# Kernel tuning notes

Hardware: AMD Instinct MI355X
Metric: run time of the kernel (lower is better)

Reference implementation:

```python
import jax, jax.numpy as jnp
import numpy as np

B, N, C = 4, 2304, 256
H = 8                      # num_heads
D = C // H                 # head_dim = 32
SCALE = D ** -0.5
H_DS, W_DS = 48, 48
UP = 2                     # spatial_down_ratio
EPS = 1e-5


def setup_inputs() -> dict:
    key = jax.random.key(0)
    ks = jax.random.split(key, 16)
    g = lambda k, shape, s: (jax.random.normal(k, shape, dtype=jnp.float32) * s)
    return {
        "x1": g(ks[0], (B, N, C), 1.0),
        "x2": g(ks[1], (B, N, C), 1.0),
        # attention projections (torch Linear convention: [out, in], no bias)
        "q1_w": g(ks[2], (C, C), C ** -0.5),
        "kv1_w": g(ks[3], (2 * C, C), C ** -0.5),
        "q2_w": g(ks[4], (C, C), C ** -0.5),
        "kv2_w": g(ks[5], (2 * C, C), C ** -0.5),
        # per-head scalar biases
        "beta12": jnp.full((H,), 0.2, dtype=jnp.float32),
        "beta21": jnp.full((H,), 0.1, dtype=jnp.float32),
        # output projections
        "p1_w": g(ks[6], (C, C), (2.0 / C) ** 0.5),
        "p1_b": g(ks[7], (C,), 1e-2),
        "p2_w": g(ks[8], (C, C), (2.0 / C) ** 0.5),
        "p2_b": g(ks[9], (C,), 1e-2),
        # LayerNorm affine params
        "g1": jnp.ones((C,), dtype=jnp.float32),
        "b1": jnp.zeros((C,), dtype=jnp.float32),
        "g2": jnp.ones((C,), dtype=jnp.float32),
        "b2": jnp.zeros((C,), dtype=jnp.float32),
    }


def _heads(x):
    # [B,N,C] -> [B,H,N,D]
    return x.reshape(B, N, H, D).transpose(0, 2, 1, 3)


def _merge(x):
    # [B,H,N,D] -> [B,N,C]
    return x.transpose(0, 2, 1, 3).reshape(B, N, C)


def _cross_attn(q, k, v, beta):
    # scores: [B,H,N,N] with per-head scalar bias
    s = jnp.einsum("bhqd,bhkd->bhqk", q, k) * SCALE + beta[None, :, None, None]
    a = jax.nn.softmax(s, axis=-1)
    return jnp.einsum("bhqk,bhkd->bhqd", a, v)


def _layernorm(x, g, b):
    mu = jnp.mean(x, axis=-1, keepdims=True)
    var = jnp.var(x, axis=-1, keepdims=True)
    return (x - mu) * jax.lax.rsqrt(var + EPS) * g + b


def _forward(x1, x2, q1_w, kv1_w, q2_w, kv2_w, beta12, beta21,
             p1_w, p1_b, p2_w, p2_b, g1, b1, g2, b2):
    q1 = _heads(x1 @ q1_w.T)
    kv1 = x1 @ kv1_w.T          # [B,N,2C]
    k1, v1 = _heads(kv1[..., :C]), _heads(kv1[..., C:])
    q2 = _heads(x2 @ q2_w.T)
    kv2 = x2 @ kv2_w.T
    k2, v2 = _heads(kv2[..., :C]), _heads(kv2[..., C:])

    o1 = _merge(_cross_attn(q1, k2, v2, beta12))   # x1 attends to x2
    o2 = _merge(_cross_attn(q2, k1, v1, beta21))   # x2 attends to x1

    y1 = _layernorm(jax.nn.relu(o1 @ p1_w.T + p1_b), g1, b1)
    y2 = _layernorm(jax.nn.relu(o2 @ p2_w.T + p2_b), g2, b2)

    # [B,N,C] -> [B,C,H_ds,W_ds]
    y1 = y1.transpose(0, 2, 1).reshape(B, C, H_DS, W_DS)
    y2 = y2.transpose(0, 2, 1).reshape(B, C, H_DS, W_DS)

    # bilinear upsample x2, align_corners=False (half-pixel == jax.image default)
    out_shape = (B, C, H_DS * UP, W_DS * UP)
    y1 = jax.image.resize(y1, out_shape, method="bilinear")
    y2 = jax.image.resize(y2, out_shape, method="bilinear")
    return y1, y2


def reference(x1, x2, q1_w, kv1_w, q2_w, kv2_w, beta12, beta21,
              p1_w, p1_b, p2_w, p2_b, g1, b1, g2, b2):
    return _forward(x1, x2, q1_w, kv1_w, q2_w, kv2_w, beta12, beta21,
                    p1_w, p1_b, p2_w, p2_b, g1, b1, g2, b2)
```

## Files before the change

kernel.cpp:

```cpp
#include <hip/hip_runtime.h>
#include <math.h>


typedef __attribute__((ext_vector_type(8))) short short8;
typedef __attribute__((ext_vector_type(4))) float f32x4;
typedef __attribute__((ext_vector_type(16))) float f32x16;
typedef __attribute__((ext_vector_type(2))) unsigned uint32x2;

#define MFMA16(a, b, c) __builtin_amdgcn_mfma_f32_16x16x32_bf16((a), (b), (c), 0, 0, 0)
#define MFMA32(a, b, c) __builtin_amdgcn_mfma_f32_32x32x16_bf16((a), (b), (c), 0, 0, 0)

__device__ __forceinline__ float bf2f(ushort u) {
    union { unsigned u; float f; } x; x.u = ((unsigned)u) << 16; return x.f;
}
__device__ __forceinline__ ushort f2bf(float f) {
    union { float f; unsigned u; } x; x.f = f;
    unsigned u = x.u;
    return (ushort)((u + 0x7fffu + ((u >> 16) & 1u)) >> 16);
}
__device__ __forceinline__ unsigned cvt_pk_bf16(float a, float b) {
    unsigned r;
    asm("v_cvt_pk_bf16_f32 %0, %1, %2" : "=v"(r) : "v"(a), "v"(b));
    return r;
}
__device__ __forceinline__ float fast_ex2(float x) {
    float r;
    asm("v_exp_f32 %0, %1" : "=v"(r) : "v"(x));
    return r;
}
__device__ __forceinline__ void plswap(unsigned &a, unsigned &b) {
    uint32x2 r = __builtin_amdgcn_permlane32_swap(a, b, false, false);
    a = r[0]; b = r[1];
}

__global__ void sniff_kernel(const ushort* __restrict__ x, int* __restrict__ flag)
{
    int lane = threadIdx.x;
    ushort u = x[lane * 2];
    int e = (u >> 7) & 0xFF;
    int outlier = (e < 100 || e > 135) ? 1 : 0;
    unsigned long long m = __ballot(outlier);
    if (lane == 0) *flag = (__popcll(m) >= 16) ? 1 : 0;
}

__global__ __launch_bounds__(256) void convert_params(
    const void* s0, const void* s1, const void* s2, const void* s3,
    const void* s4, const void* s5, const void* s6, const void* s7,
    const void* s8, const void* s9, const void* s10, const void* s11,
    ushort* __restrict__ dst, const int* __restrict__ flag)
{
    int idx = blockIdx.x * 256 + threadIdx.x;
    if (idx >= 525824) return;
    const void* src; int off;
    if      (idx < 65536)  { src = s0;  off = idx; }
    else if (idx < 196608) { src = s1;  off = idx - 65536; }
    else if (idx < 262144) { src = s2;  off = idx - 196608; }
    else if (idx < 393216) { src = s3;  off = idx - 262144; }
    else if (idx < 458752) { src = s4;  off = idx - 393216; }
    else if (idx < 524288) { src = s5;  off = idx - 458752; }
    else if (idx < 524544) { src = s6;  off = idx - 524288; }
    else if (idx < 524800) { src = s7;  off = idx - 524544; }
    else if (idx < 525056) { src = s8;  off = idx - 524800; }
    else if (idx < 525312) { src = s9;  off = idx - 525056; }
    else if (idx < 525568) { src = s10; off = idx - 525312; }
    else                   { src = s11; off = idx - 525568; }
    ushort v = (*flag) ? f2bf(((const float*)src)[off])
                       : ((const ushort*)src)[off];
    dst[idx] = v;
}

__global__ __launch_bounds__(256) void convert_x(
    const void* __restrict__ x1, const void* __restrict__ x2,
    ushort* __restrict__ o1, ushort* __restrict__ o2,
    const int* __restrict__ flag)
{
    int idx = blockIdx.x * 256 + threadIdx.x;
    int which = idx >= 294912;
    int off = (which ? idx - 294912 : idx) * 8;
    const void* src = which ? x2 : x1;
    ushort* dst = which ? o2 : o1;
    if (*flag) {
        const float* p = (const float*)src + off;
        float4 a = *(const float4*)p;
        float4 c = *(const float4*)(p + 4);
        uint4 u;
        u.x = cvt_pk_bf16(a.x, a.y);
        u.y = cvt_pk_bf16(a.z, a.w);
        u.z = cvt_pk_bf16(c.x, c.y);
        u.w = cvt_pk_bf16(c.z, c.w);
        *(uint4*)(dst + off) = u;
    } else {
        *(uint4*)(dst + off) = *(const uint4*)((const ushort*)src + off);
    }
}

__global__ __launch_bounds__(256) void gemm_bt(
    const void* __restrict__ Ain, const ushort* __restrict__ W,
    ushort* __restrict__ C, const ushort* __restrict__ bias,
    int M, int N, int K, int relu, const int* __restrict__ dflag, int a_ext,
    int mode, ushort* __restrict__ Kh, ushort* __restrict__ Vt,
    const ushort* __restrict__ W2, const ushort* __restrict__ bias2,
    ushort* __restrict__ Kh2, ushort* __restrict__ Vt2, int mhalf)
{
    __shared__ __align__(16) ushort As[64][40];
    __shared__ __align__(16) ushort Ws[64][40];

    const int m0 = blockIdx.x * 64;
    const int n0 = blockIdx.y * 64;
    const int tid = threadIdx.x;
    const int w = tid >> 6;
    const int lane = tid & 63;
    const int lm = lane & 15;
    const int quad = lane >> 4;
    const int a32 = a_ext ? *dflag : 0;

    const int side = (mhalf && m0 >= mhalf) ? 1 : 0;
    const ushort* Wu = side ? W2 : W;
    const ushort* bu = side ? bias2 : bias;
    ushort* Khu = side ? Kh2 : Kh;
    ushort* Vtu = side ? Vt2 : Vt;

    const f32x4 Z4 = {0.f, 0.f, 0.f, 0.f};
    f32x4 acc[4];
    for (int j = 0; j < 4; j++) acc[j] = Z4;

    const ushort* A16 = (const ushort*)Ain;
    const float*  A32 = (const float*)Ain;
    const int row = tid >> 2, off = (tid & 3) * 8;

    for (int k0 = 0; k0 < K; k0 += 32) {
        __syncthreads();
        if (a32) {
            const float* p0 = A32 + (size_t)(m0 + row) * K + k0 + off;
            float4 f0 = *(const float4*)p0;
            float4 f1 = *(const float4*)(p0 + 4);
            uint4 t0;
            t0.x = cvt_pk_bf16(f0.x, f0.y);
            t0.y = cvt_pk_bf16(f0.z, f0.w);
            t0.z = cvt_pk_bf16(f1.x, f1.y);
            t0.w = cvt_pk_bf16(f1.z, f1.w);
            *(uint4*)&As[row][off] = t0;
        } else {
            *(uint4*)&As[row][off] =
                *(const uint4*)(A16 + (size_t)(m0 + row) * K + k0 + off);
        }
        *(uint4*)&Ws[row][off] =
            *(const uint4*)(Wu + (size_t)(n0 + row) * K + k0 + off);
        __syncthreads();

        short8 af = *(const short8*)&As[w * 16 + lm][quad * 8];
        for (int nt = 0; nt < 4; nt++) {
            short8 wf = *(const short8*)&Ws[nt * 16 + lm][quad * 8];
            acc[nt] = MFMA16(af, wf, acc[nt]);
        }
    }

    const int grow = m0 + w * 16 + quad * 4;
    const int grel = grow - (side ? mhalf : 0);
    if (mode == 1) {
        const float QSC = 0.17677669529663687f * 1.4426950408889634f;
        int bb = grel / 2304;
        int tok = grel - bb * 2304;
        for (int nt = 0; nt < 4; nt++) {
            int col = n0 + nt * 16 + lm;
            if (col < 256) {
                for (int r = 0; r < 4; r++)
                    C[(size_t)(grow + r) * 256 + col] = f2bf(acc[nt][r] * QSC);
            } else if (col < 512) {
                int c2 = col - 256, hh = c2 >> 5, d = c2 & 31;
                size_t kb = ((size_t)(bb * 8 + hh) * 72 + (tok >> 5)) * 1024
                          + (size_t)(d >> 4) * 512 + (size_t)(d & 15);
                for (int r = 0; r < 4; r++)
                    Khu[kb + (size_t)((tok + r) & 31) * 16] = f2bf(acc[nt][r]);
            } else {
                int c2 = col - 512, hh = c2 >> 5, d = c2 & 31;
                size_t vb = ((size_t)(bb * 8 + hh) * 144 + (tok >> 4)) * 512
                          + (size_t)d * 16 + (size_t)(tok & 15);
                uint2 o;
                o.x = cvt_pk_bf16(acc[nt][0], acc[nt][1]);
                o.y = cvt_pk_bf16(acc[nt][2], acc[nt][3]);
                *(uint2*)&Vtu[vb] = o;
            }
        }
    } else {
        for (int nt = 0; nt < 4; nt++) {
            int col = n0 + nt * 16 + lm;
            float bv = bu ? bf2f(bu[col]) : 0.f;
            for (int r = 0; r < 4; r++) {
                float v = acc[nt][r] + bv;
                if (relu) v = fmaxf(v, 0.f);
                C[(size_t)(grow + r) * N + col] = f2bf(v);
            }
        }
    }
}

__global__ __launch_bounds__(256) void attn_kernel(
    const ushort* __restrict__ Qa, const ushort* __restrict__ Kha,
    const ushort* __restrict__ Vta, ushort* __restrict__ Oa,
    const ushort* __restrict__ Qb, const ushort* __restrict__ Khb2,
    const ushort* __restrict__ Vtb2, ushort* __restrict__ Ob)
{
    __shared__ float Lo[4][2][64][16];
    __shared__ float Ll[4][2][64];

    const int sid = blockIdx.x;
    const int qb = blockIdx.y;
    const int side = sid >> 5;
    const int bh = sid & 31;
    const ushort* Q  = side ? Qb   : Qa;
    const ushort* Kh = side ? Khb2 : Kha;
    const ushort* Vt = side ? Vtb2 : Vta;
    ushort* O        = side ? Ob   : Oa;

    const int b = bh >> 3, h = bh & 7;
    const int tid = threadIdx.x;
    const int w = tid >> 6, lane = tid & 63;
    const int l31 = lane & 31, hl = lane >> 5;

    const int qrow0 = qb * 64 + l31;
    const int qrow1 = qrow0 + 32;
    const ushort* qp0 = Q + ((size_t)b * 2304 + qrow0) * 256 + h * 32 + hl * 8;
    const ushort* qp1 = Q + ((size_t)b * 2304 + qrow1) * 256 + h * 32 + hl * 8;
    const short8 qf0a = *(const short8*)qp0;
    const short8 qf1a = *(const short8*)(qp0 + 16);
    const short8 qf0b = *(const short8*)qp1;
    const short8 qf1b = *(const short8*)(qp1 + 16);

    f32x16 oa, ob;
    #pragma unroll
    for (int i = 0; i < 16; i++) { oa[i] = 0.f; ob[i] = 0.f; }
    const f32x16 Z16 = oa;
    float la = 0.f, lb = 0.f;

    const ushort* kp0 = Kh + (size_t)bh * 73728 + l31 * 16 + hl * 8;
    const ushort* vp0 = Vt + (size_t)bh * 73728 + l31 * 16 + hl * 8;

#define LOADT(kf0v, kf1v, vf0v, vf1v, t) { \
    const ushort* _kp = kp0 + (size_t)(t) * 1024; \
    kf0v = *(const short8*)_kp; \
    kf1v = *(const short8*)(_kp + 512); \
    const ushort* _vp = vp0 + (size_t)(t) * 1024; \
    vf0v = *(const short8*)_vp; \
    vf1v = *(const short8*)(_vp + 512); \
}
#define QSET(kf0v, kf1v, vf0v, vf1v, qf0v, qf1v, oacc, lacc) { \
    f32x16 s = MFMA32(kf0v, qf0v, Z16); \
    s = MFMA32(kf1v, qf1v, s); \
    float p[16]; \
    _Pragma("unroll") \
    for (int i = 0; i < 16; i++) p[i] = fast_ex2(s[i]); \
    lacc += (((p[0] + p[1]) + (p[2] + p[3])) + ((p[4] + p[5]) + (p[6] + p[7]))) \
          + (((p[8] + p[9]) + (p[10] + p[11])) + ((p[12] + p[13]) + (p[14] + p[15]))); \
    unsigned c0 = cvt_pk_bf16(p[0],  p[1]); \
    unsigned c1 = cvt_pk_bf16(p[2],  p[3]); \
    unsigned c2 = cvt_pk_bf16(p[4],  p[5]); \
    unsigned c3 = cvt_pk_bf16(p[6],  p[7]); \
    unsigned c4 = cvt_pk_bf16(p[8],  p[9]); \
    unsigned c5 = cvt_pk_bf16(p[10], p[11]); \
    unsigned c6 = cvt_pk_bf16(p[12], p[13]); \
    unsigned c7 = cvt_pk_bf16(p[14], p[15]); \
    plswap(c0, c2); plswap(c1, c3); plswap(c4, c6); plswap(c5, c7); \
    union { unsigned u[4]; short8 s8; } pA, pB; \
    pA.u[0] = c0; pA.u[1] = c1; pA.u[2] = c2; pA.u[3] = c3; \
    pB.u[0] = c4; pB.u[1] = c5; pB.u[2] = c6; pB.u[3] = c7; \
    oacc = MFMA32(vf0v, pA.s8, oacc); \
    oacc = MFMA32(vf1v, pB.s8, oacc); \
}
#define COMP(kf0v, kf1v, vf0v, vf1v) { \
    QSET(kf0v, kf1v, vf0v, vf1v, qf0a, qf1a, oa, la); \
    QSET(kf0v, kf1v, vf0v, vf1v, qf0b, qf1b, ob, lb); \
}

    short8 kA0, kA1, vA0, vA1;
    short8 kB0, kB1, vB0, vB1;

    const int t0 = w * 18;

    LOADT(kA0, kA1, vA0, vA1, t0);
    LOADT(kB0, kB1, vB0, vB1, t0 + 1);

    for (int i = 0; i < 9; i++) {
        COMP(kA0, kA1, vA0, vA1);
        { int ta = t0 + 2 * i + 2; ta = ta < 72 ? ta : 70;
          LOADT(kA0, kA1, vA0, vA1, ta); }
        COMP(kB0, kB1, vB0, vB1);
        { int tb = t0 + 2 * i + 3; tb = tb < 72 ? tb : 71;
          LOADT(kB0, kB1, vB0, vB1, tb); }
    }
#undef LOADT
#undef QSET
#undef COMP

    la += __shfl_xor(la, 32, 64);
    lb += __shfl_xor(lb, 32, 64);

    #pragma unroll
    for (int r = 0; r < 16; r++) {
        Lo[w][0][lane][r] = oa[r];
        Lo[w][1][lane][r] = ob[r];
    }
    Ll[w][0][lane] = la;
    Ll[w][1][lane] = lb;
    __syncthreads();

    if (w < 2) {
        float os[16];
        #pragma unroll
        for (int r = 0; r < 16; r++) os[r] = 0.f;
        float ls = 0.f;
        #pragma unroll
        for (int u = 0; u < 4; u++) {
            ls += Ll[u][w][lane];
            #pragma unroll
            for (int r = 0; r < 16; r++) os[r] += Lo[u][w][lane][r];
        }
        float rl = 1.f / ls;
        const int qrow = (w == 0) ? qrow0 : qrow1;
        ushort* op = O + ((size_t)b * 2304 + qrow) * 256 + h * 32 + hl * 4;
        #pragma unroll
        for (int g = 0; g < 4; g++) {
            uint2 o;
            o.x = cvt_pk_bf16(os[4 * g] * rl, os[4 * g + 1] * rl);
            o.y = cvt_pk_bf16(os[4 * g + 2] * rl, os[4 * g + 3] * rl);
            *(uint2*)(op + 8 * g) = o;
        }
    }
}

__global__ __launch_bounds__(256) void lnt_kernel(
    const ushort* __restrict__ Z, const ushort* __restrict__ G1,
    const ushort* __restrict__ B1, const ushort* __restrict__ G2,
    const ushort* __restrict__ B2, ushort* __restrict__ Yt)
{
    __shared__ ushort T[256][72];

    const int tid = threadIdx.x;
    const int tok0 = blockIdx.x * 32;
    const int half = (tok0 >= 9216) ? 1 : 0;
    const int tr = tok0 - half * 9216;
    const int bb = tr / 2304;
    const int tokb = tr - bb * 2304;

    const int tok_l = tid >> 3;
    const int cq = tid & 7;

    const ushort* zp = Z + ((size_t)(tok0 + tok_l)) * 256 + cq * 32;
    uint dd[16];
    for (int i = 0; i < 4; i++) {
        uint4 v = *(const uint4*)(zp + i * 8);
        dd[i * 4 + 0] = v.x; dd[i * 4 + 1] = v.y;
        dd[i * 4 + 2] = v.z; dd[i * 4 + 3] = v.w;
    }
    float s = 0.f, q = 0.f;
    for (int e = 0; e < 16; e++) {
        float x0 = bf2f((ushort)dd[e]);
        float x1 = bf2f((ushort)(dd[e] >> 16));
        s += x0 + x1;
        q += x0 * x0 + x1 * x1;
    }
    s += __shfl_xor(s, 1, 64); q += __shfl_xor(q, 1, 64);
    s += __shfl_xor(s, 2, 64); q += __shfl_xor(q, 2, 64);
    s += __shfl_xor(s, 4, 64); q += __shfl_xor(q, 4, 64);
    float mu = s * (1.f / 256.f);
    float var = q * (1.f / 256.f) - mu * mu;
    float rs = rsqrtf(var + 1e-5f);

    const ushort* Gs = half ? G2 : G1;
    const ushort* Bs = half ? B2 : B1;
    const int col = tok_l + 4 * cq;

    for (int i = 0; i < 4; i++) {
        int cb = cq * 32 + i * 8;
        uint4 gv = *(const uint4*)(Gs + cb);
        uint4 bv = *(const uint4*)(Bs + cb);
        uint gg[4] = {gv.x, gv.y, gv.z, gv.w};
        uint bw[4] = {bv.x, bv.y, bv.z, bv.w};
        for (int k = 0; k < 4; k++) {
            uint u = dd[i * 4 + k];
            float x0 = bf2f((ushort)u), x1 = bf2f((ushort)(u >> 16));
            float y0 = (x0 - mu) * rs * bf2f((ushort)gg[k]) + bf2f((ushort)bw[k]);
            float y1 = (x1 - mu) * rs * bf2f((ushort)(gg[k] >> 16))
                     + bf2f((ushort)(bw[k] >> 16));
            int c = cb + 2 * k;
            T[c][col]     = f2bf(y0);
            T[c + 1][col] = f2bf(y1);
        }
    }
    __syncthreads();

    const int c_row = tid >> 3;
    const int tq = (tid & 7) * 4;
    const size_t obase = ((size_t)((half * 4 + bb) * 256)) * 2304 + tokb + tq;
    for (int i = 0; i < 8; i++) {
        int c = c_row + 32 * i;
        uint2 v = *(const uint2*)&T[c][tq + 4 * i];
        *(uint2*)(Yt + obase + (size_t)c * 2304) = v;
    }
}

__global__ __launch_bounds__(256) void upsample_kernel(
    const ushort* __restrict__ Yt, float* __restrict__ out)
{
    int idx = blockIdx.x * 256 + threadIdx.x;
    int m  = idx % 48;
    int t  = idx / 48;
    int oi = t % 96;
    int bc = t / 96;

    float fi = oi * 0.5f - 0.25f;
    int i0 = (int)floorf(fi);
    float wi = fi - (float)i0;
    int i1 = i0 + 1 < 47 ? i0 + 1 : 47;
    i0 = i0 > 0 ? i0 : 0;
    int jm = m - 1 > 0 ? m - 1 : 0;
    int jp = m + 1 < 47 ? m + 1 : 47;

    const ushort* r0 = Yt + (size_t)bc * 2304 + i0 * 48;
    const ushort* r1 = Yt + (size_t)bc * 2304 + i1 * 48;
    float a0 = bf2f(r0[jm]), b0 = bf2f(r0[m]), c0 = bf2f(r0[jp]);
    float a1 = bf2f(r1[jm]), b1 = bf2f(r1[m]), c1 = bf2f(r1[jp]);
    float u = 1.f - wi;
    float ha = u * a0 + wi * a1;
    float hb = u * b0 + wi * b1;
    float hc = u * c0 + wi * c1;
    float2 o;
    o.x = 0.25f * ha + 0.75f * hb;
    o.y = 0.75f * hb + 0.25f * hc;
    *(float2*)(out + (size_t)bc * 9216 + oi * 96 + m * 2) = o;
}

extern "C" void kernel_launch(void* const* d_in, const int* in_sizes, int n_in,
                              void* d_out, int out_size, void* d_ws, size_t ws_size,
                              hipStream_t stream)
{
    (void)in_sizes; (void)n_in; (void)out_size; (void)ws_size;

    ushort* ws  = (ushort*)d_ws;
    ushort* Q1  = ws;
    ushort* Q2  = Q1  + 2359296;
    ushort* KV1 = Q2  + 2359296;
    ushort* KV2 = KV1 + 4718592;
    ushort* wc  = KV2 + 4718592;
    int*    dflag = (int*)(wc + 525824);

    ushort* cqkv1w = wc;
    ushort* cqkv2w = wc + 196608;
    ushort* cp1w  = wc + 393216;
    ushort* cp2w  = wc + 458752;
    ushort* cp1b  = wc + 524288;
    ushort* cp2b  = wc + 524544;
    ushort* cg1   = wc + 524800;
    ushort* cb1   = wc + 525056;
    ushort* cg2   = wc + 525312;
    ushort* cb2   = wc + 525568;

    float*  outf = (float*)d_out;
    ushort* O1  = (ushort*)d_out;
    ushort* O2  = O1 + 2359296;
    ushort* Xb1 = O2 + 2359296;
    ushort* Xb2 = Xb1 + 2359296;
    ushort* Z1  = KV2;
    ushort* Yt  = Q1;
    (void)Q2; (void)O2; (void)Xb2;

    dim3 blk(256);
    sniff_kernel<<<dim3(1), dim3(64), 0, stream>>>((const ushort*)d_in[0], dflag);
    convert_params<<<dim3(2054), blk, 0, stream>>>(
        d_in[2], d_in[3], d_in[4], d_in[5], d_in[8], d_in[10],
        d_in[9], d_in[11], d_in[12], d_in[13], d_in[14], d_in[15],
        wc, dflag);
    convert_x<<<dim3(2304), blk, 0, stream>>>(d_in[0], d_in[1], Xb1, Xb2, dflag);

    gemm_bt<<<dim3(288, 12), blk, 0, stream>>>(Xb1, cqkv1w, Q1, nullptr,
        18432, 768, 256, 0, dflag, 0, 1, KV1, KV1 + 2359296,
        cqkv2w, nullptr, KV2, KV2 + 2359296, 9216);

    attn_kernel<<<dim3(64, 36), dim3(256), 0, stream>>>(
        Q1, KV2, KV2 + 2359296, O1,
        Q2, KV1, KV1 + 2359296, O2);

    gemm_bt<<<dim3(288, 4), blk, 0, stream>>>(O1, cp1w, Z1, cp1b,
        18432, 256, 256, 1, dflag, 0, 0, nullptr, nullptr,
        cp2w, cp2b, nullptr, nullptr, 9216);

    lnt_kernel<<<dim3(576), blk, 0, stream>>>(Z1, cg1, cb1, cg2, cb2, Yt);

    upsample_kernel<<<dim3(36864), blk, 0, stream>>>(Yt, outf);
}
```

Baseline: 247.2 us.

## Enlarge GEMM block tile to 128x128 with 4x4 MFMA tiles per wave

New measurement: 249.6 us. No clear change (+1.0%).

```diff
diff --git a/kernel.cpp b/kernel.cpp
--- a/kernel.cpp
+++ b/kernel.cpp
@@ -102,13 +102,14 @@
     const ushort* __restrict__ W2, const ushort* __restrict__ bias2,
     ushort* __restrict__ Kh2, ushort* __restrict__ Vt2, int mhalf)
 {
-    __shared__ __align__(16) ushort As[64][40];
-    __shared__ __align__(16) ushort Ws[64][40];
-
-    const int m0 = blockIdx.x * 64;
-    const int n0 = blockIdx.y * 64;
+    __shared__ __align__(16) ushort As[128][40];
+    __shared__ __align__(16) ushort Ws[128][40];
+
+    const int m0 = blockIdx.x * 128;
+    const int n0 = blockIdx.y * 128;
     const int tid = threadIdx.x;
     const int w = tid >> 6;
+    const int wr = w >> 1, wc = w & 1;
     const int lane = tid & 63;
     const int lm = lane & 15;
     const int quad = lane >> 4;
@@ -121,75 +122,103 @@
     ushort* Vtu = side ? Vt2 : Vt;
 
     const f32x4 Z4 = {0.f, 0.f, 0.f, 0.f};
-    f32x4 acc[4];
-    for (int j = 0; j < 4; j++) acc[j] = Z4;
+    f32x4 acc[4][4];
+    for (int i = 0; i < 4; i++)
+        for (int j = 0; j < 4; j++) acc[i][j] = Z4;
 
     const ushort* A16 = (const ushort*)Ain;
     const float*  A32 = (const float*)Ain;
-    const int row = tid >> 2, off = (tid & 3) * 8;
+    const int row = tid >> 1, off16 = (tid & 1) * 16;
 
     for (int k0 = 0; k0 < K; k0 += 32) {
         __syncthreads();
         if (a32) {
-            const float* p0 = A32 + (size_t)(m0 + row) * K + k0 + off;
+            const float* p0 = A32 + (size_t)(m0 + row) * K + k0 + off16;
             float4 f0 = *(const float4*)p0;
             float4 f1 = *(const float4*)(p0 + 4);
-            uint4 t0;
+            float4 f2 = *(const float4*)(p0 + 8);
+            float4 f3 = *(const float4*)(p0 + 12);
+            uint4 t0, t1;
             t0.x = cvt_pk_bf16(f0.x, f0.y);
             t0.y = cvt_pk_bf16(f0.z, f0.w);
             t0.z = cvt_pk_bf16(f1.x, f1.y);
             t0.w = cvt_pk_bf16(f1.z, f1.w);
-            *(uint4*)&As[row][off] = t0;
+            t1.x = cvt_pk_bf16(f2.x, f2.y);
+            t1.y = cvt_pk_bf16(f2.z, f2.w);
+            t1.z = cvt_pk_bf16(f3.x, f3.y);
+            t1.w = cvt_pk_bf16(f3.z, f3.w);
+            *(uint4*)&As[row][off16]     = t0;
+            *(uint4*)&As[row][off16 + 8] = t1;
         } else {
-            *(uint4*)&As[row][off] =
-                *(const uint4*)(A16 + (size_t)(m0 + row) * K + k0 + off);
-        }
-        *(uint4*)&Ws[row][off] =
-            *(const uint4*)(Wu + (size_t)(n0 + row) * K + k0 + off);
+            const ushort* p0 = A16 + (size_t)(m0 + row) * K + k0 + off16;
+            *(uint4*)&As[row][off16]     = *(const uint4*)p0;
+            *(uint4*)&As[row][off16 + 8] = *(const uint4*)(p0 + 8);
+        }
+        {
+            const ushort* p0 = Wu + (size_t)(n0 + row) * K + k0 + off16;
+            *(uint4*)&Ws[row][off16]     = *(const uint4*)p0;
+            *(uint4*)&Ws[row][off16 + 8] = *(const uint4*)(p0 + 8);
+        }
         __syncthreads();
 
-        short8 af = *(const short8*)&As[w * 16 + lm][quad * 8];
-        for (int nt = 0; nt < 4; nt++) {
-            short8 wf = *(const short8*)&Ws[nt * 16 + lm][quad * 8];
-            acc[nt] = MFMA16(af, wf, acc[nt]);
-        }
-    }
-
-    const int grow = m0 + w * 16 + quad * 4;
-    const int grel = grow - (side ? mhalf : 0);
+        short8 af[4], wf[4];
+        #pragma unroll
+        for (int mt = 0; mt < 4; mt++)
+            af[mt] = *(const short8*)&As[wr * 64 + mt * 16 + lm][quad * 8];
+        #pragma unroll
+        for (int nt = 0; nt < 4; nt++)
+            wf[nt] = *(const short8*)&Ws[wc * 64 + nt * 16 + lm][quad * 8];
+        #pragma unroll
+        for (int mt = 0; mt < 4; mt++)
+            #pragma unroll
+            for (int nt = 0; nt < 4; nt++)
+                acc[mt][nt] = MFMA16(af[mt], wf[nt], acc[mt][nt]);
+    }
+
     if (mode == 1) {
         const float QSC = 0.17677669529663687f * 1.4426950408889634f;
-        int bb = grel / 2304;
-        int tok = grel - bb * 2304;
-        for (int nt = 0; nt < 4; nt++) {
-            int col = n0 + nt * 16 + lm;
-            if (col < 256) {
-                for (int r = 0; r < 4; r++)
-                    C[(size_t)(grow + r) * 256 + col] = f2bf(acc[nt][r] * QSC);
-            } else if (col < 512) {
-                int c2 = col - 256, hh = c2 >> 5, d = c2 & 31;
-                size_t kb = ((size_t)(bb * 8 + hh) * 72 + (tok >> 5)) * 1024
-                          + (size_t)(d >> 4) * 512 + (size_t)(d & 15);
-                for (int r = 0; r < 4; r++)
-                    Khu[kb + (size_t)((tok + r) & 31) * 16] = f2bf(acc[nt][r]);
-            } else {
-                int c2 = col - 512, hh = c2 >> 5, d = c2 & 31;
-                size_t vb = ((size_t)(bb * 8 + hh) * 144 + (tok >> 4)) * 512
-                          + (size_t)d * 16 + (size_t)(tok & 15);
-                uint2 o;
-                o.x = cvt_pk_bf16(acc[nt][0], acc[nt][1]);
-                o.y = cvt_pk_bf16(acc[nt][2], acc[nt][3]);
-                *(uint2*)&Vtu[vb] = o;
+        #pragma unroll
+        for (int mt = 0; mt < 4; mt++) {
+            const int grow = m0 + wr * 64 + mt * 16 + quad * 4;
+            const int grel = grow - (side ? mhalf : 0);
+            int bb = grel / 2304;
+            int tok = grel - bb * 2304;
+            #pragma unroll
+            for (int nt = 0; nt < 4; nt++) {
+                int col = n0 + wc * 64 + nt * 16 + lm;
+                if (col < 256) {
+                    for (int r = 0; r < 4; r++)
+                        C[(size_t)(grow + r) * 256 + col] = f2bf(acc[mt][nt][r] * QSC);
+                } else if (col < 512) {
+                    int c2 = col - 256, hh = c2 >> 5, d = c2 & 31;
+                    size_t kb = ((size_t)(bb * 8 + hh) * 72 + (tok >> 5)) * 1024
+                              + (size_t)(d >> 4) * 512 + (size_t)(d & 15);
+                    for (int r = 0; r < 4; r++)
+                        Khu[kb + (size_t)((tok + r) & 31) * 16] = f2bf(acc[mt][nt][r]);
+                } else {
+                    int c2 = col - 512, hh = c2 >> 5, d = c2 & 31;
+                    size_t vb = ((size_t)(bb * 8 + hh) * 144 + (tok >> 4)) * 512
+                              + (size_t)d * 16 + (size_t)(tok & 15);
+                    uint2 o;
+                    o.x = cvt_pk_bf16(acc[mt][nt][0], acc[mt][nt][1]);
+                    o.y = cvt_pk_bf16(acc[mt][nt][2], acc[mt][nt][3]);
+                    *(uint2*)&Vtu[vb] = o;
+                }
             }
         }
     } else {
-        for (int nt = 0; nt < 4; nt++) {
-            int col = n0 + nt * 16 + lm;
-            float bv = bu ? bf2f(bu[col]) : 0.f;
-            for (int r = 0; r < 4; r++) {
-                float v = acc[nt][r] + bv;
-                if (relu) v = fmaxf(v, 0.f);
-                C[(size_t)(grow + r) * N + col] = f2bf(v);
+        #pragma unroll
+        for (int mt = 0; mt < 4; mt++) {
+            const int grow = m0 + wr * 64 + mt * 16 + quad * 4;
+            #pragma unroll
+            for (int nt = 0; nt < 4; nt++) {
+                int col = n0 + wc * 64 + nt * 16 + lm;
+                float bv = bu ? bf2f(bu[col]) : 0.f;
+                for (int r = 0; r < 4; r++) {
+                    float v = acc[mt][nt][r] + bv;
+                    if (relu) v = fmaxf(v, 0.f);
+                    C[(size_t)(grow + r) * N + col] = f2bf(v);
+                }
             }
         }
     }
@@ -472,7 +501,7 @@
         wc, dflag);
     convert_x<<<dim3(2304), blk, 0, stream>>>(d_in[0], d_in[1], Xb1, Xb2, dflag);
 
-    gemm_bt<<<dim3(288, 12), blk, 0, stream>>>(Xb1, cqkv1w, Q1, nullptr,
+    gemm_bt<<<dim3(144, 6), blk, 0, stream>>>(Xb1, cqkv1w, Q1, nullptr,
         18432, 768, 256, 0, dflag, 0, 1, KV1, KV1 + 2359296,
         cqkv2w, nullptr, KV2, KV2 + 2359296, 9216);
 
@@ -480,7 +509,7 @@
         Q1, KV2, KV2 + 2359296, O1,
         Q2, KV1, KV1 + 2359296, O2);
 
-    gemm_bt<<<dim3(288, 4), blk, 0, stream>>>(O1, cp1w, Z1, cp1b,
+    gemm_bt<<<dim3(144, 2), blk, 0, stream>>>(O1, cp1w, Z1, cp1b,
         18432, 256, 256, 1, dflag, 0, 0, nullptr, nullptr,
         cp2w, cp2b, nullptr, nullptr, 9216);
 
```
